# Kernel tuning notes

Measured on AMD Instinct MI355X. Metric: run time of the kernel, lower is better.

## Reference

```python
import jax, jax.numpy as jnp
import numpy as np

V, E, H = 32000, 256, 512   # vocab, embed_dim, hidden_dim
B, S, T = 16, 512, 128      # batch, src_len, tgt_len
PAD = 0
H2 = 2 * H                  # decoder hidden size


def setup_inputs() -> dict:
    key = jax.random.key(0)
    ks = jax.random.split(key, 20)
    g = lambda k, shape: jax.random.normal(k, shape, dtype=jnp.float32) * 0.05
    emb = g(ks[0], (V, E)).at[PAD].set(0.0)  # padding_idx row zeroed
    inp = {
        "src": jax.random.randint(ks[18], (B, S), 0, V, dtype=jnp.int32),
        "tgt": jax.random.randint(ks[19], (B, T), 0, V, dtype=jnp.int32),
        "emb": emb,
        # encoder forward direction (torch gate order i,f,g,o)
        "Wih_f": g(ks[1], (4 * H, E)), "Whh_f": g(ks[2], (4 * H, H)),
        "bih_f": g(ks[3], (4 * H,)),   "bhh_f": g(ks[4], (4 * H,)),
        # encoder backward direction
        "Wih_b": g(ks[5], (4 * H, E)), "Whh_b": g(ks[6], (4 * H, H)),
        "bih_b": g(ks[7], (4 * H,)),   "bhh_b": g(ks[8], (4 * H,)),
        # decoder LSTM: input E+2H, hidden 2H
        "Wih_d": g(ks[9], (4 * H2, E + H2)), "Whh_d": g(ks[10], (4 * H2, H2)),
        "bih_d": g(ks[11], (4 * H2,)),       "bhh_d": g(ks[12], (4 * H2,)),
        # attention Linear(4H -> 2H)
        "Wa": g(ks[13], (H2, 2 * H2)), "ba": g(ks[14], (H2,)),
        # output Linear(2H -> V)
        "Wo": g(ks[15], (V, H2)), "bo": g(ks[16], (V,)),
    }
    return inp


def _lstm_cell(x, h, c, Wih, Whh, bih, bhh):
    z = x @ Wih.T + h @ Whh.T + bih + bhh
    i, f, g, o = jnp.split(z, 4, axis=-1)
    c = jax.nn.sigmoid(f) * c + jax.nn.sigmoid(i) * jnp.tanh(g)
    h = jax.nn.sigmoid(o) * jnp.tanh(c)
    return h, c


def _lstm_scan(xs, h0, c0, Wih, Whh, bih, bhh):
    def step(carry, x):
        h, c = _lstm_cell(x, carry[0], carry[1], Wih, Whh, bih, bhh)
        return (h, c), h
    (hT, cT), hs = jax.lax.scan(step, (h0, c0), xs)
    return hs, hT, cT


def reference(src, tgt, emb, Wih_f, Whh_f, bih_f, bhh_f, Wih_b, Whh_b, bih_b, bhh_b,
              Wih_d, Whh_d, bih_d, bhh_d, Wa, ba, Wo, bo):
    z = jnp.zeros((B, H), dtype=emb.dtype)
    xs = emb[src].transpose(1, 0, 2)                       # [S,B,E]
    hs_f, hTf, _ = _lstm_scan(xs,        z, z, Wih_f, Whh_f, bih_f, bhh_f)
    hs_b, hTb, _ = _lstm_scan(xs[::-1],  z, z, Wih_b, Whh_b, bih_b, bhh_b)
    enc_out = jnp.concatenate([hs_f, hs_b[::-1]], -1).transpose(1, 0, 2)  # [B,S,2H]
    h = jnp.concatenate([hTf, hTb], -1)                    # decoder h0 [B,2H]
    c = jnp.zeros_like(h)  # note: original reuses encoder c_n; see combined c0 below
    # original uses c_n (last cells) as decoder c0:
    _, _, cTf = _lstm_scan(xs, z, z, Wih_f, Whh_f, bih_f, bhh_f)[1], None, None
    # recompute cleanly (scan already returned cT above; redo properly):
    hs_f2, hTf2, cTf2 = _lstm_scan(xs,       z, z, Wih_f, Whh_f, bih_f, bhh_f)
    hs_b2, hTb2, cTb2 = _lstm_scan(xs[::-1], z, z, Wih_b, Whh_b, bih_b, bhh_b)
    c = jnp.concatenate([cTf2, cTb2], -1)

    Wa_h, Wa_e = Wa[:, :H2], Wa[:, H2:]
    enc_proj = jnp.einsum('bsd,kd->bsk', enc_out, Wa_e) + ba  # [B,S,2H]

    dec_xs = emb[tgt[:, :T - 1]].transpose(1, 0, 2)        # [T-1,B,E] teacher-forced

    def dec_step(carry, x):
        h, c = carry
        energy = jnp.tanh(enc_proj + (h @ Wa_h.T)[:, None, :])  # [B,S,2H]
        w = jax.nn.softmax(energy.sum(-1), axis=1)              # [B,S]
        ctx = jnp.einsum('bs,bsd->bd', w, enc_out)              # [B,2H]
        xi = jnp.concatenate([x, ctx], -1)                      # [B,E+2H]
        h, c = _lstm_cell(xi, h, c, Wih_d, Whh_d, bih_d, bhh_d)
        pred = h @ Wo.T + bo                                    # [B,V]
        return (h, c), pred

    _, preds = jax.lax.scan(dec_step, (h, c), dec_xs)           # [T-1,B,V]
    outputs = jnp.concatenate(
        [jnp.zeros((B, 1, V), dtype=preds.dtype), preds.transpose(1, 0, 2)], axis=1)
    return outputs
```

## Files before the change

### kernel.cpp

```cpp
#include <hip/hip_runtime.h>

typedef unsigned int uint;
typedef unsigned short ushort;
typedef unsigned long long ull;
typedef __attribute__((ext_vector_type(8))) short bf16x8;
typedef __attribute__((ext_vector_type(4))) float f32x4;

static constexpr int V_ = 32000, E_ = 256, H_ = 512, B_ = 16, S_ = 512, T_ = 128;
static constexpr int H2_ = 1024, G4_ = 2048, D4_ = 4096, KXI_ = 2304;
static constexpr int DSTEPS = T_ - 1;
static constexpr int MD = 2048;
static constexpr int NWG_DEC = 256;
static constexpr float LOG2E = 1.4426950408889634f;
static constexpr int ASTR = 2312;

#define DEVFN __device__ __forceinline__

DEVFN ushort f2bf(float f){ uint u = __builtin_bit_cast(uint, f); u += 0x7fffu + ((u>>16)&1u); return (ushort)(u>>16); }
DEVFN float bf2f(ushort h){ uint u = ((uint)h)<<16; return __builtin_bit_cast(float, u); }
DEVFN float fsig(float x){ float e = __builtin_amdgcn_exp2f(-LOG2E*x); return __builtin_amdgcn_rcpf(1.f+e); }
DEVFN float ftanh(float x){ x = fminf(15.f,fmaxf(-15.f,x)); float e = __builtin_amdgcn_exp2f(2.f*LOG2E*x); return (e-1.f)*__builtin_amdgcn_rcpf(e+1.f); }
DEVFN f32x4 mfma16(bf16x8 a, bf16x8 b, f32x4 c){ return __builtin_amdgcn_mfma_f32_16x16x32_bf16(a,b,c,0,0,0); }

struct ull2v{ ull x, y; };
DEVFN ull ald64(const void* p){ return __hip_atomic_load((const ull*)p, __ATOMIC_RELAXED, __HIP_MEMORY_SCOPE_AGENT); }
DEVFN uint ald32u(const uint* p){ return __hip_atomic_load(p, __ATOMIC_RELAXED, __HIP_MEMORY_SCOPE_AGENT); }
DEVFN float ald_f32(const float* p){ uint v = __hip_atomic_load((const uint*)p, __ATOMIC_RELAXED, __HIP_MEMORY_SCOPE_AGENT); return __builtin_bit_cast(float, v); }
DEVFN bf16x8 ald_bf16x8(const ushort* p){ ull2v v{ald64(p), ald64(p+4)}; return __builtin_bit_cast(bf16x8, v); }
DEVFN void ast32(float* p, float v){ __hip_atomic_store(p, v, __ATOMIC_RELAXED, __HIP_MEMORY_SCOPE_AGENT); }
DEVFN void ast16(ushort* p, ushort v){ __hip_atomic_store(p, v, __ATOMIC_RELAXED, __HIP_MEMORY_SCOPE_AGENT); }
DEVFN void astu(uint* p, uint v){ __hip_atomic_store(p, v, __ATOMIC_RELAXED, __HIP_MEMORY_SCOPE_AGENT); }

DEVFN void gbar(uint* flags, int wgid, int tid, uint& rnd){
  __syncthreads();
  rnd++;
  if (tid==0) astu(flags + wgid, rnd);
  if (tid<256){
    while (ald32u(flags + tid) < rnd) __builtin_amdgcn_s_sleep(1);
  }
  __syncthreads();
}
DEVFN void lbar(uint* lflags, int grp, int mem, int tid, uint& rnd){
  __syncthreads();
  rnd++;
  if (tid==0) astu(lflags + grp*16 + mem, rnd);
  if (tid<16){
    while (ald32u(lflags + grp*16 + tid) < rnd) __builtin_amdgcn_s_sleep(1);
  }
  __syncthreads();
}

__global__ void k_init(uint* __restrict__ flags, ushort* __restrict__ hgf, ushort* __restrict__ hgb,
                       uint* __restrict__ hU, uint* __restrict__ ctxU){
  int i = blockIdx.x*256 + threadIdx.x;
  if (i < 1024) flags[i] = 0;
  if (i < 2*B_*H_){ hgf[i]=0; hgb[i]=0; }
  if (i < B_*H2_){ hU[i] = 0u; ctxU[i] = 0u; }
}

__global__ void k_embed(const int* __restrict__ src, const int* __restrict__ tgt,
                        const float* __restrict__ emb, ushort* __restrict__ Xb, ushort* __restrict__ DXb){
  int r = blockIdx.x, tid = threadIdx.x;
  if (r < S_*B_){
    int s = r>>4, b = r&15;
    int id = src[b*S_+s];
    Xb[(size_t)r*E_+tid] = f2bf(emb[(size_t)id*E_+tid]);
  } else {
    int r2 = r - S_*B_;
    int t = r2>>4, b = r2&15;
    int id = tgt[b*T_+t];
    DXb[(size_t)r2*E_+tid] = f2bf(emb[(size_t)id*E_+tid]);
  }
}

__global__ void k_cvt_encw(const float* __restrict__ src, ushort* __restrict__ dst){
  int d = blockIdx.x;
  int wg = d>>7, r = d&127;
  int w = r>>4, jj=(r>>2)&3, g=r&3;
  int srow = g*H_ + wg*32 + w*4 + jj;
  for (int c = threadIdx.x; c < E_; c += 256)
    dst[(size_t)d*E_ + c] = f2bf(src[(size_t)srow*E_ + c]);
}

__global__ void k_bias_encp(const float* __restrict__ bih, const float* __restrict__ bhh, float* __restrict__ dst){
  int d = blockIdx.x*256 + threadIdx.x;
  int wg = d>>7, r = d&127;
  int w = r>>4, jj=(r>>2)&3, g=r&3;
  int srow = g*H_ + wg*32 + w*4 + jj;
  dst[d] = bih[srow]+bhh[srow];
}

__global__ void k_cvt_decw(const float* __restrict__ Wih_d, const float* __restrict__ Whh_d,
                           ushort* __restrict__ dst){
  int d = blockIdx.x;
  int wg = d>>4, r = d&15, jj = r>>2, g = r&3;
  int srow = g*H2_ + wg*4 + jj;
  for (int c = threadIdx.x; c < KXI_; c += 256){
    float v = (c < E_+H2_) ? Wih_d[(size_t)srow*(E_+H2_) + c] : Whh_d[(size_t)srow*H2_ + (c - (E_+H2_))];
    dst[(size_t)d*KXI_ + c] = f2bf(v);
  }
}

__global__ void k_bias_decp(const float* __restrict__ bih, const float* __restrict__ bhh, float* __restrict__ dst){
  int d = blockIdx.x*256 + threadIdx.x;
  int wg = d>>4, r = d&15, jj = r>>2, g = r&3;
  int srow = g*H2_ + wg*4 + jj;
  dst[d] = bih[srow]+bhh[srow];
}

__global__ void k_cvt_strided(const float* __restrict__ src, ushort* __restrict__ dst,
                              int cols, int sld, int soff, int dld, int doff){
  int r = blockIdx.x;
  for (int c = threadIdx.x; c < cols; c += 256)
    dst[(size_t)r*dld + doff + c] = f2bf(src[(size_t)r*sld + soff + c]);
}

__global__ void k_zero_t0(float* __restrict__ out){
  int i = blockIdx.x*256 + threadIdx.x;
  if (i < B_*V_){ int b = i / V_, v = i - b*V_; out[(size_t)b*T_*V_ + v] = 0.f; }
}

template<int MODE>
__global__ __launch_bounds__(256) void gemm128(const ushort* __restrict__ A, const ushort* __restrict__ Bm,
    const float* __restrict__ bias, void* __restrict__ outp, int M, int N, int K, int Mvalid){
  __shared__ __align__(16) ushort As[128*32];
  __shared__ __align__(16) ushort Bs[128*32];
  int tid = threadIdx.x;
  int wave = tid>>6, lane = tid&63;
  int m0 = blockIdx.y*128, n0 = blockIdx.x*128;
  int wm = wave>>1, wn = wave&1;
  int col = lane&15, rg = lane>>4;
  f32x4 acc[4][4];
  #pragma unroll
  for (int i=0;i<4;i++)
    #pragma unroll
    for (int j=0;j<4;j++) acc[i][j] = {0.f,0.f,0.f,0.f};
  for (int k0=0;k0<K;k0+=32){
    __syncthreads();
    #pragma unroll
    for (int j=0;j<2;j++){
      int li = j*256+tid;
      int row = li>>2, ko = (li&3)*8;
      *(bf16x8*)(As + li*8) = *(const bf16x8*)(A + (size_t)(m0+row)*K + k0 + ko);
      *(bf16x8*)(Bs + li*8) = *(const bf16x8*)(Bm + (size_t)(n0+row)*K + k0 + ko);
    }
    __syncthreads();
    bf16x8 af[4], bfr[4];
    #pragma unroll
    for (int f=0;f<4;f++){
      af[f]  = *(const bf16x8*)(As + (wm*64+f*16+col)*32 + rg*8);
      bfr[f] = *(const bf16x8*)(Bs + (wn*64+f*16+col)*32 + rg*8);
    }
    #pragma unroll
    for (int fm=0;fm<4;fm++)
      #pragma unroll
      for (int fn=0;fn<4;fn++)
        acc[fm][fn] = mfma16(af[fm], bfr[fn], acc[fm][fn]);
  }
  #pragma unroll
  for (int fm=0;fm<4;fm++){
    int mrow = m0 + wm*64 + fm*16 + rg*4;
    #pragma unroll
    for (int fn=0;fn<4;fn++){
      int gcol = n0 + wn*64 + fn*16 + col;
      float bv = bias ? bias[gcol] : 0.f;
      #pragma unroll
      for (int i=0;i<4;i++){
        float v = acc[fm][fn][i] + bv;
        int grow = mrow + i;
        if (MODE==0) ((float*)outp)[(size_t)grow*N + gcol] = v;
        else if (MODE==1) ((ushort*)outp)[(size_t)grow*N + gcol] = f2bf(v);
        else if (MODE==3) ((ushort*)outp)[(size_t)(grow>>4)*(16*2048) + gcol*16 + (grow&15)] = f2bf(v);
        else { if (grow < Mvalid){ int b = grow&15, t = grow>>4;
               ((float*)outp)[(size_t)b*T_*V_ + (size_t)(t+1)*V_ + gcol] = v; } }
      }
    }
  }
}

__global__ __launch_bounds__(512) void k_enc_persist(
    const ushort* __restrict__ Xgf, const ushort* __restrict__ Xgb,
    const float* __restrict__ Whhf, const float* __restrict__ Whhb,
    ushort* __restrict__ enc, ushort* __restrict__ enct,
    uint* __restrict__ hbuf1, float* __restrict__ cbuf0,
    ushort* __restrict__ hgf, ushort* __restrict__ hgb,
    uint* __restrict__ flags){
  const int dir = blockIdx.x >> 4;
  const int wg  = blockIdx.x & 15;
  const ushort* Xg = dir ? Xgb : Xgf;
  const float* Whh = dir ? Whhb : Whhf;
  ushort* hg = dir ? hgb : hgf;
  uint* ef = flags + 512 + dir*16;
  __shared__ __align__(16) ushort Wlds[128*512];
  __shared__ __align__(16) ushort hls[16*512];
  int tid = threadIdx.x;
  for (int it=0; it<32; ++it){
    int r = it*4 + (tid>>7), ct = tid&127;
    int w_ = r>>4, jj=(r>>2)&3, g=r&3;
    int srow = g*H_ + wg*32 + w_*4 + jj;
    float4 v = *(const float4*)(Whh + (size_t)srow*H_ + ct*4);
    ushort4 o; o.x=f2bf(v.x); o.y=f2bf(v.y); o.z=f2bf(v.z); o.w=f2bf(v.w);
    int byte = (r*1024 + ct*8) ^ ((r&7)<<4);
    *(ushort4*)((char*)Wlds + byte) = o;
  }
  int w = tid>>6, lane = tid&63, colL = lane&15, rg = lane>>4;
  int gg = colL&3;
  uint rnd = 0;
  float cst[4];
  #pragma unroll
  for (int i=0;i<4;i++) cst[i]=0.f;
  __syncthreads();
  for (int t=0;t<S_;++t){
    int pos = dir ? (S_-1-t) : t;
    const ushort* hsrc = hg + (t&1)*B_*H_;
    bf16x8 hv[2];
    #pragma unroll
    for (int k2=0;k2<2;k2++){
      int idx = tid + k2*512;
      hv[k2] = ald_bf16x8(hsrc + (idx>>6)*H_ + (idx&63)*8);
    }
    int colg = wg*128 + w*16 + colL;
    ushort4 xv = *(const ushort4*)(Xg + ((size_t)pos*2048 + colg)*16 + rg*4);
    f32x4 acc;
    acc[0]=bf2f(xv.x); acc[1]=bf2f(xv.y); acc[2]=bf2f(xv.z); acc[3]=bf2f(xv.w);
    #pragma unroll
    for (int k2=0;k2<2;k2++){
      int idx = tid + k2*512;
      int byte = ((idx>>6)*1024 + (idx&63)*16) ^ (((idx>>6)&7)<<4);
      *(bf16x8*)((char*)hls + byte) = hv[k2];
    }
    __syncthreads();
    int rowb = w*16 + colL;
    int base = rowb*1024 + rg*16, xm = (rowb&7)<<4;
    int hbase = colL*1024 + rg*16, hxm = (colL&7)<<4;
    #pragma unroll
    for (int kt=0;kt<16;kt++){
      bf16x8 afv = *(const bf16x8*)((const char*)hls + ((hbase + kt*64) ^ hxm));
      bf16x8 bfv = *(const bf16x8*)((const char*)Wlds + ((base + kt*64) ^ xm));
      acc = mfma16(afv, bfv, acc);
    }
    ushort* hdst = hg + ((t+1)&1)*B_*H_;
    #pragma unroll
    for (int i=0;i<4;i++){
      float v0 = acc[i];
      float v1 = __shfl_xor(v0, 1);
      float v2 = __shfl_xor(v0, 2);
      float v3 = __shfl_xor(v1, 2);
      float zi = gg==0?v0: gg==1?v1: gg==2?v2: v3;
      float zf = (gg^1)==0?v0: (gg^1)==1?v1: (gg^1)==2?v2: v3;
      float zg = (gg^2)==0?v0: (gg^2)==1?v1: (gg^2)==2?v2: v3;
      float zo = (gg^3)==0?v0: (gg^3)==1?v1: (gg^3)==2?v2: v3;
      float cc = fsig(zf)*cst[i] + fsig(zi)*ftanh(zg);
      cst[i] = cc;
      float h = fsig(zo)*ftanh(cc);
      if (gg==0){
        int j = wg*32 + w*4 + (colL>>2);
        int b = rg*4+i;
        ushort hb = f2bf(h);
        enc[((size_t)b*S_ + pos)*H2_ + dir*H_ + j] = hb;
        enct[((size_t)b*H2_ + dir*H_ + j)*S_ + pos] = hb;
        ast16(&hdst[b*H_ + j], hb);
        if (t==S_-1){
          hbuf1[b*H2_ + dir*H_ + j] = (uint)hb;
          cbuf0[b*H2_ + dir*H_ + j] = cc;
        }
      }
    }
    if (t != S_-1){
      __syncthreads();
      rnd++;
      if (tid==0) astu(ef + wg, rnd);
      if (tid<16){
        while (ald32u(ef + tid) < rnd) __builtin_amdgcn_s_sleep(1);
      }
      __syncthreads();
    }
  }
}

__global__ __launch_bounds__(512) void k_dec(
    const float* __restrict__ P, const ushort* __restrict__ WaH,
    const ushort* __restrict__ Wd, const float* __restrict__ bsd,
    const ushort* __restrict__ enct, const ushort* __restrict__ DXb,
    const float* __restrict__ cbuf0, uint* __restrict__ hU,
    uint* __restrict__ ctxU, float* __restrict__ qbuf,
    float* __restrict__ scores, ushort* __restrict__ hsd,
    uint* __restrict__ flags){
  __shared__ __align__(16) ushort AB[16*ASTR];
  __shared__ __align__(16) float pr[8*256];
  __shared__ float redz[256];
  __shared__ float qls[1024];
  __shared__ float wls[512];
  __shared__ float part[512];
  __shared__ float red[16];
  __shared__ float cst[64];
  uint* lflags = flags + 256;
  int wgid = blockIdx.x, tid = threadIdx.x;
  int w = tid>>6, lane = tid&63, colL = lane&15, rg = lane>>4;
  int b = wgid>>4, wc = wgid&15;
  uint rnd = 0;
  if (tid < 64){
    int jj = tid>>4, b4 = tid&15;
    cst[tid] = cbuf0[b4*H2_ + wgid*4 + jj];
  }
  for (int st=0; st<DSTEPS; ++st){
    const uint* hprevU = hU + ((st+1)&1)*B_*H2_;
    const uint wantH = (uint)st;
    const uint wantC = (uint)(st+1);
    float* qslot = qbuf + (st&1)*B_*H2_;
    if (wgid >= 64 && wgid < 128){
      int n0 = (wgid-64)*16;
      const uint* hp = hprevU + colL*H2_ + w*128 + rg*8;
      uint uu[32];
      for(;;){
        #pragma unroll
        for (int kt=0;kt<4;kt++)
          #pragma unroll
          for (int j=0;j<4;j++){
            ull v = ald64(hp + kt*32 + j*2);
            uu[kt*8+j*2] = (uint)v; uu[kt*8+j*2+1] = (uint)(v>>32);
          }
        bool ok = true;
        #pragma unroll
        for (int i2=0;i2<32;i2++) ok &= ((uu[i2]>>16) == wantH);
        if (ok) break;
        __builtin_amdgcn_s_sleep(1);
      }
      f32x4 acc = {0.f,0.f,0.f,0.f};
      const ushort* Bp = WaH + (size_t)(n0+colL)*H2_ + w*128 + rg*8;
      #pragma unroll
      for (int kt=0;kt<4;kt++){
        ushort tmp[8];
        #pragma unroll
        for (int j=0;j<8;j++) tmp[j] = (ushort)uu[kt*8+j];
        acc = mfma16(*(bf16x8*)tmp, *(const bf16x8*)(Bp + kt*32), acc);
      }
      *(f32x4*)&pr[w*256 + lane*4] = acc;
      __syncthreads();
      if (tid < 256){
        float s = pr[tid];
        #pragma unroll
        for (int w8=1;w8<8;w8++) s += pr[w8*256 + tid];
        int l = tid>>2, i = tid&3;
        ast32(&qslot[(size_t)((l>>4)*4 + i)*H2_ + n0 + (l&15)], s);
      }
    }
    gbar(flags, wgid, tid, rnd);
    {
      ull q2 = ald64((const ull*)(qslot + (size_t)b*H2_) + tid);
      *(ull*)&qls[tid*2] = q2;
      __syncthreads();
      f32x4 qv[4];
      #pragma unroll
      for (int u=0;u<4;u++) qv[u] = *(const f32x4*)&qls[lane*16 + u*4];
      int rbase = b*S_ + wc*32 + w*4;
      #pragma unroll
      for (int rr=0;rr<4;rr++){
        int r = rbase + rr;
        const float4* Pr = (const float4*)(P + (size_t)r*H2_) + lane*4;
        float s = 0.f;
        #pragma unroll
        for (int u=0;u<4;u++){
          float4 pv = Pr[u];
          s += ftanh(pv.x+qv[u][0])+ftanh(pv.y+qv[u][1])+ftanh(pv.z+qv[u][2])+ftanh(pv.w+qv[u][3]);
        }
        #pragma unroll
        for (int o=32;o;o>>=1) s += __shfl_xor(s,o);
        if (lane==0) ast32(&scores[r], s);
      }
    }
    lbar(lflags, b, wc, tid, rnd);
    {
      float sc = ald_f32(scores + b*S_ + tid);
      float m = sc;
      #pragma unroll
      for (int o=32;o;o>>=1) m = fmaxf(m, __shfl_xor(m,o));
      if (lane==0) red[w] = m;
      __syncthreads();
      m = red[0];
      #pragma unroll
      for (int k2=1;k2<8;k2++) m = fmaxf(m, red[k2]);
      float e = __builtin_amdgcn_exp2f((sc - m)*LOG2E);
      float ss = e;
      #pragma unroll
      for (int o=32;o;o>>=1) ss += __shfl_xor(ss,o);
      if (lane==0) red[8+w] = ss;
      __syncthreads();
      float tot = red[8];
      #pragma unroll
      for (int k2=9;k2<16;k2++) tot += red[k2];
      wls[tid] = e * __builtin_amdgcn_rcpf(tot);
      __syncthreads();
      int c = wc*64 + (tid&63), sseg = tid>>6;
      const ushort* ep = enct + ((size_t)b*H2_ + c)*S_ + sseg*64;
      float a = 0.f;
      #pragma unroll
      for (int u=0;u<8;u++){
        bf16x8 ev = *(const bf16x8*)(ep + u*8);
        #pragma unroll
        for (int j=0;j<8;j++) a += wls[sseg*64 + u*8 + j] * bf2f((ushort)ev[j]);
      }
      part[tid] = a;
      __syncthreads();
      if (tid < 64){
        float s = part[tid];
        #pragma unroll
        for (int g2=1;g2<8;g2++) s += part[g2*64 + tid];
        astu(&ctxU[b*H2_ + wc*64 + tid], (uint)f2bf(s) | (wantC<<16));
      }
    }
    {
      { int b3 = tid>>5, seg = tid&31;
        *(bf16x8*)&AB[b3*ASTR + seg*8] = *(const bf16x8*)(DXb + (size_t)(st*16+b3)*E_ + seg*8); }
      {
        uint uu[32];
        for(;;){
          #pragma unroll
          for (int k2=0;k2<4;k2++){
            int idx = tid + k2*512;
            const uint* p = ctxU + (idx>>7)*H2_ + (idx&127)*8;
            #pragma unroll
            for (int j=0;j<4;j++){
              ull v = ald64(p + j*2);
              uu[k2*8+j*2] = (uint)v; uu[k2*8+j*2+1] = (uint)(v>>32);
            }
          }
          bool ok = true;
          #pragma unroll
          for (int i2=0;i2<32;i2++) ok &= ((uu[i2]>>16) == wantC);
          if (ok) break;
          __builtin_amdgcn_s_sleep(1);
        }
        #pragma unroll
        for (int k2=0;k2<4;k2++){
          int idx = tid + k2*512;
          ushort tmp[8];
          #pragma unroll
          for (int j=0;j<8;j++) tmp[j] = (ushort)uu[k2*8+j];
          *(bf16x8*)&AB[(idx>>7)*ASTR + 256 + (idx&127)*8] = *(bf16x8*)tmp;
        }
      }
      {
        uint uu[32];
        for(;;){
          #pragma unroll
          for (int k2=0;k2<4;k2++){
            int idx = tid + k2*512;
            const uint* p = hprevU + (idx>>7)*H2_ + (idx&127)*8;
            #pragma unroll
            for (int j=0;j<4;j++){
              ull v = ald64(p + j*2);
              uu[k2*8+j*2] = (uint)v; uu[k2*8+j*2+1] = (uint)(v>>32);
            }
          }
          bool ok = true;
          #pragma unroll
          for (int i2=0;i2<32;i2++) ok &= ((uu[i2]>>16) == wantH);
          if (ok) break;
          __builtin_amdgcn_s_sleep(1);
        }
        #pragma unroll
        for (int k2=0;k2<4;k2++){
          int idx = tid + k2*512;
          ushort tmp[8];
          #pragma unroll
          for (int j=0;j<8;j++) tmp[j] = (ushort)uu[k2*8+j];
          *(bf16x8*)&AB[(idx>>7)*ASTR + 1280 + (idx&127)*8] = *(bf16x8*)tmp;
        }
      }
      __syncthreads();
      int row0 = wgid*16;
      f32x4 acc = {0.f,0.f,0.f,0.f};
      const ushort* Bp = Wd + (size_t)(row0+colL)*KXI_ + w*288 + rg*8;
      const ushort* Apb = &AB[colL*ASTR + w*288 + rg*8];
      #pragma unroll
      for (int kt=0;kt<9;kt++)
        acc = mfma16(*(const bf16x8*)(Apb + kt*32), *(const bf16x8*)(Bp + kt*32), acc);
      *(f32x4*)&pr[w*256 + lane*4] = acc;
      __syncthreads();
      if (tid < 256){
        float s = bsd[row0 + ((tid>>2)&15)];
        #pragma unroll
        for (int w8=0;w8<8;w8++) s += pr[w8*256 + tid];
        redz[tid] = s;
      }
      __syncthreads();
      if (tid < 64){
        int jj = tid>>4, b4 = tid&15, rgc = b4>>2, ic = b4&3;
        float zi = redz[((jj*4+0) + 16*rgc)*4 + ic];
        float zf = redz[((jj*4+1) + 16*rgc)*4 + ic];
        float zg = redz[((jj*4+2) + 16*rgc)*4 + ic];
        float zo = redz[((jj*4+3) + 16*rgc)*4 + ic];
        float cc2 = fsig(zf)*cst[tid] + fsig(zi)*ftanh(zg);
        cst[tid] = cc2;
        float h = fsig(zo)*ftanh(cc2);
        ushort hb = f2bf(h);
        int j = wgid*4 + jj;
        astu(&hU[(st&1)*B_*H2_ + b4*H2_ + j], (uint)hb | ((uint)(st+1)<<16));
        hsd[((size_t)st*B_ + b4)*H2_ + j] = hb;
      }
      __syncthreads();
    }
  }
}

extern "C" void kernel_launch(void* const* d_in, const int* in_sizes, int n_in,
                              void* d_out, int out_size, void* d_ws, size_t ws_size,
                              hipStream_t stream) {
  const int* src   = (const int*)d_in[0];
  const int* tgt   = (const int*)d_in[1];
  const float* emb   = (const float*)d_in[2];
  const float* Wih_f = (const float*)d_in[3];
  const float* Whh_f = (const float*)d_in[4];
  const float* bih_f = (const float*)d_in[5];
  const float* bhh_f = (const float*)d_in[6];
  const float* Wih_b = (const float*)d_in[7];
  const float* Whh_b = (const float*)d_in[8];
  const float* bih_b = (const float*)d_in[9];
  const float* bhh_b = (const float*)d_in[10];
  const float* Wih_d = (const float*)d_in[11];
  const float* Whh_d = (const float*)d_in[12];
  const float* bih_d = (const float*)d_in[13];
  const float* bhh_d = (const float*)d_in[14];
  const float* Wa    = (const float*)d_in[15];
  const float* ba    = (const float*)d_in[16];
  const float* Wo    = (const float*)d_in[17];
  const float* bo    = (const float*)d_in[18];
  float* out = (float*)d_out;
  (void)in_sizes; (void)n_in; (void)out_size; (void)ws_size;

  char* ws = (char*)d_ws;
  size_t off = 0;
  auto alloc = [&](size_t bytes)->char*{ char* p = ws + off; off += (bytes + 255) & ~(size_t)255; return p; };
  ushort* Xb     = (ushort*)alloc((size_t)S_*B_*E_*2);
  ushort* DXb    = (ushort*)alloc((size_t)DSTEPS*B_*E_*2);
  ushort* Wihf_p = (ushort*)alloc((size_t)G4_*E_*2);
  ushort* Wihb_p = (ushort*)alloc((size_t)G4_*E_*2);
  float*  bsf    = (float*)alloc(G4_*4);
  float*  bsb    = (float*)alloc(G4_*4);
  ushort* ENC    = (ushort*)alloc((size_t)B_*S_*H2_*2);
  ushort* ENCT   = (ushort*)alloc((size_t)B_*S_*H2_*2);
  ushort* WaH    = (ushort*)alloc((size_t)H2_*H2_*2);
  ushort* WaE    = (ushort*)alloc((size_t)H2_*H2_*2);
  ushort* Wd     = (ushort*)alloc((size_t)D4_*KXI_*2);
  float*  bsd    = (float*)alloc(D4_*4);
  ushort* WoB    = (ushort*)alloc((size_t)V_*H2_*2);
  float*  cbuf0  = (float*)alloc(B_*H2_*4);
  uint*   hU     = (uint*)alloc((size_t)2*B_*H2_*4);
  uint*   ctxU   = (uint*)alloc((size_t)B_*H2_*4);
  float*  qbuf   = (float*)alloc((size_t)2*B_*H2_*4);
  float*  scores = (float*)alloc(B_*S_*4);
  ushort* hsd    = (ushort*)alloc((size_t)MD*H2_*2);
  ushort* hgf    = (ushort*)alloc((size_t)2*B_*H_*2);
  ushort* hgb    = (ushort*)alloc((size_t)2*B_*H_*2);
  uint*   flags  = (uint*)alloc(4096);
  char*   big    = alloc((size_t)2*S_*B_*G4_*2);
  ushort* Xgf = (ushort*)big;
  ushort* Xgb = (ushort*)(big + (size_t)S_*B_*G4_*2);
  float*  P   = (float*)big;

  k_init<<<dim3(64), dim3(256), 0, stream>>>(flags, hgf, hgb, hU, ctxU);
  k_embed<<<dim3(S_*B_ + DSTEPS*B_), dim3(E_), 0, stream>>>(src, tgt, emb, Xb, DXb);
  k_cvt_encw<<<dim3(G4_), dim3(256), 0, stream>>>(Wih_f, Wihf_p);
  k_cvt_encw<<<dim3(G4_), dim3(256), 0, stream>>>(Wih_b, Wihb_p);
  k_bias_encp<<<dim3(8), dim3(256), 0, stream>>>(bih_f, bhh_f, bsf);
  k_bias_encp<<<dim3(8), dim3(256), 0, stream>>>(bih_b, bhh_b, bsb);
  k_cvt_strided<<<dim3(H2_), dim3(256), 0, stream>>>(Wa, WaH, H2_, 2*H2_, 0,   H2_, 0);
  k_cvt_strided<<<dim3(H2_), dim3(256), 0, stream>>>(Wa, WaE, H2_, 2*H2_, H2_, H2_, 0);
  k_cvt_decw<<<dim3(D4_), dim3(256), 0, stream>>>(Wih_d, Whh_d, Wd);
  k_bias_decp<<<dim3(16), dim3(256), 0, stream>>>(bih_d, bhh_d, bsd);
  k_cvt_strided<<<dim3(V_),  dim3(256), 0, stream>>>(Wo, WoB, H2_, H2_, 0, H2_, 0);

  gemm128<3><<<dim3(G4_/128, (S_*B_)/128), dim3(256), 0, stream>>>(Xb, Wihf_p, bsf, Xgf, S_*B_, G4_, E_, 0);
  gemm128<3><<<dim3(G4_/128, (S_*B_)/128), dim3(256), 0, stream>>>(Xb, Wihb_p, bsb, Xgb, S_*B_, G4_, E_, 0);

  k_enc_persist<<<dim3(32), dim3(512), 0, stream>>>(Xgf, Xgb, Whh_f, Whh_b, ENC, ENCT,
                                                    hU + B_*H2_, cbuf0, hgf, hgb, flags);

  gemm128<0><<<dim3(H2_/128, (B_*S_)/128), dim3(256), 0, stream>>>(ENC, WaE, ba, P, B_*S_, H2_, H2_, 0);
  k_zero_t0<<<dim3((B_*V_+255)/256), dim3(256), 0, stream>>>(out);

  k_dec<<<dim3(NWG_DEC), dim3(512), 0, stream>>>(P, WaH, Wd, bsd, ENCT, DXb, cbuf0, hU,
                                                 ctxU, qbuf, scores, hsd, flags);

  gemm128<2><<<dim3(V_/128, MD/128), dim3(256), 0, stream>>>(hsd, WoB, bo, out, MD, V_, H2_, DSTEPS*B_);
}
```

Before: 6.039 ms.

## Replace step barriers with tagged-data polling in encoder and decoder

The encoder stops using a flag barrier across its 16 workgroups after every step. Each hidden value is now stored as a 32-bit word holding the step number in its upper half, and consumers poll until every word they read carries the expected tag. In the decoder, the full 256-workgroup barrier after the query projection is replaced by waiting only on the 64 producer workgroups' flags, and the context buffer is double-buffered so a slot can be reused safely. This removes global barrier round-trips on the serial critical path, at the cost of doubling the hidden-state traffic and adding spin-polling on data.

```diff
diff --git a/kernel.cpp b/kernel.cpp
--- a/kernel.cpp
+++ b/kernel.cpp
@@ -26,20 +26,10 @@
 DEVFN ull ald64(const void* p){ return __hip_atomic_load((const ull*)p, __ATOMIC_RELAXED, __HIP_MEMORY_SCOPE_AGENT); }
 DEVFN uint ald32u(const uint* p){ return __hip_atomic_load(p, __ATOMIC_RELAXED, __HIP_MEMORY_SCOPE_AGENT); }
 DEVFN float ald_f32(const float* p){ uint v = __hip_atomic_load((const uint*)p, __ATOMIC_RELAXED, __HIP_MEMORY_SCOPE_AGENT); return __builtin_bit_cast(float, v); }
-DEVFN bf16x8 ald_bf16x8(const ushort* p){ ull2v v{ald64(p), ald64(p+4)}; return __builtin_bit_cast(bf16x8, v); }
 DEVFN void ast32(float* p, float v){ __hip_atomic_store(p, v, __ATOMIC_RELAXED, __HIP_MEMORY_SCOPE_AGENT); }
 DEVFN void ast16(ushort* p, ushort v){ __hip_atomic_store(p, v, __ATOMIC_RELAXED, __HIP_MEMORY_SCOPE_AGENT); }
 DEVFN void astu(uint* p, uint v){ __hip_atomic_store(p, v, __ATOMIC_RELAXED, __HIP_MEMORY_SCOPE_AGENT); }
 
-DEVFN void gbar(uint* flags, int wgid, int tid, uint& rnd){
-  __syncthreads();
-  rnd++;
-  if (tid==0) astu(flags + wgid, rnd);
-  if (tid<256){
-    while (ald32u(flags + tid) < rnd) __builtin_amdgcn_s_sleep(1);
-  }
-  __syncthreads();
-}
 DEVFN void lbar(uint* lflags, int grp, int mem, int tid, uint& rnd){
   __syncthreads();
   rnd++;
@@ -50,12 +40,13 @@
   __syncthreads();
 }
 
-__global__ void k_init(uint* __restrict__ flags, ushort* __restrict__ hgf, ushort* __restrict__ hgb,
+__global__ void k_init(uint* __restrict__ flags, uint* __restrict__ hgf, uint* __restrict__ hgb,
                        uint* __restrict__ hU, uint* __restrict__ ctxU){
   int i = blockIdx.x*256 + threadIdx.x;
   if (i < 1024) flags[i] = 0;
-  if (i < 2*B_*H_){ hgf[i]=0; hgb[i]=0; }
-  if (i < B_*H2_){ hU[i] = 0u; ctxU[i] = 0u; }
+  if (i < 2*B_*H_){ hgf[i]=0u; hgb[i]=0u; }
+  if (i < B_*H2_) hU[i] = 0u;
+  if (i < 2*B_*H2_) ctxU[i] = 0u;
 }
 
 __global__ void k_embed(const int* __restrict__ src, const int* __restrict__ tgt,
@@ -183,14 +174,12 @@
     const float* __restrict__ Whhf, const float* __restrict__ Whhb,
     ushort* __restrict__ enc, ushort* __restrict__ enct,
     uint* __restrict__ hbuf1, float* __restrict__ cbuf0,
-    ushort* __restrict__ hgf, ushort* __restrict__ hgb,
-    uint* __restrict__ flags){
+    uint* __restrict__ hgf, uint* __restrict__ hgb){
   const int dir = blockIdx.x >> 4;
   const int wg  = blockIdx.x & 15;
   const ushort* Xg = dir ? Xgb : Xgf;
   const float* Whh = dir ? Whhb : Whhf;
-  ushort* hg = dir ? hgb : hgf;
-  uint* ef = flags + 512 + dir*16;
+  uint* hg = dir ? hgb : hgf;
   __shared__ __align__(16) ushort Wlds[128*512];
   __shared__ __align__(16) ushort hls[16*512];
   int tid = threadIdx.x;
@@ -205,19 +194,30 @@
   }
   int w = tid>>6, lane = tid&63, colL = lane&15, rg = lane>>4;
   int gg = colL&3;
-  uint rnd = 0;
   float cst[4];
   #pragma unroll
   for (int i=0;i<4;i++) cst[i]=0.f;
   __syncthreads();
   for (int t=0;t<S_;++t){
     int pos = dir ? (S_-1-t) : t;
-    const ushort* hsrc = hg + (t&1)*B_*H_;
-    bf16x8 hv[2];
-    #pragma unroll
-    for (int k2=0;k2<2;k2++){
-      int idx = tid + k2*512;
-      hv[k2] = ald_bf16x8(hsrc + (idx>>6)*H_ + (idx&63)*8);
+    const uint* hsrcU = hg + (t&1)*B_*H_;
+    uint uu[16];
+    for(;;){
+      #pragma unroll
+      for (int k2=0;k2<2;k2++){
+        int idx = tid + k2*512;
+        const uint* p = hsrcU + (idx>>6)*H_ + (idx&63)*8;
+        #pragma unroll
+        for (int j=0;j<4;j++){
+          ull v = ald64(p + j*2);
+          uu[k2*8+j*2] = (uint)v; uu[k2*8+j*2+1] = (uint)(v>>32);
+        }
+      }
+      bool ok = true;
+      #pragma unroll
+      for (int i2=0;i2<16;i2++) ok &= ((uu[i2]>>16) == (uint)t);
+      if (ok) break;
+      __builtin_amdgcn_s_sleep(1);
     }
     int colg = wg*128 + w*16 + colL;
     ushort4 xv = *(const ushort4*)(Xg + ((size_t)pos*2048 + colg)*16 + rg*4);
@@ -227,7 +227,10 @@
     for (int k2=0;k2<2;k2++){
       int idx = tid + k2*512;
       int byte = ((idx>>6)*1024 + (idx&63)*16) ^ (((idx>>6)&7)<<4);
-      *(bf16x8*)((char*)hls + byte) = hv[k2];
+      ushort tmp[8];
+      #pragma unroll
+      for (int j=0;j<8;j++) tmp[j] = (ushort)uu[k2*8+j];
+      *(bf16x8*)((char*)hls + byte) = *(bf16x8*)tmp;
     }
     __syncthreads();
     int rowb = w*16 + colL;
@@ -239,7 +242,7 @@
       bf16x8 bfv = *(const bf16x8*)((const char*)Wlds + ((base + kt*64) ^ xm));
       acc = mfma16(afv, bfv, acc);
     }
-    ushort* hdst = hg + ((t+1)&1)*B_*H_;
+    uint* hdstU = hg + ((t+1)&1)*B_*H_;
     #pragma unroll
     for (int i=0;i<4;i++){
       float v0 = acc[i];
@@ -259,22 +262,14 @@
         ushort hb = f2bf(h);
         enc[((size_t)b*S_ + pos)*H2_ + dir*H_ + j] = hb;
         enct[((size_t)b*H2_ + dir*H_ + j)*S_ + pos] = hb;
-        ast16(&hdst[b*H_ + j], hb);
+        astu(&hdstU[b*H_ + j], (uint)hb | ((uint)(t+1)<<16));
         if (t==S_-1){
           hbuf1[b*H2_ + dir*H_ + j] = (uint)hb;
           cbuf0[b*H2_ + dir*H_ + j] = cc;
         }
       }
     }
-    if (t != S_-1){
-      __syncthreads();
-      rnd++;
-      if (tid==0) astu(ef + wg, rnd);
-      if (tid<16){
-        while (ald32u(ef + tid) < rnd) __builtin_amdgcn_s_sleep(1);
-      }
-      __syncthreads();
-    }
+    __syncthreads();
   }
 }
 
@@ -295,6 +290,7 @@
   __shared__ float red[16];
   __shared__ float cst[64];
   uint* lflags = flags + 256;
+  uint* qf     = flags + 768;
   int wgid = blockIdx.x, tid = threadIdx.x;
   int w = tid>>6, lane = tid&63, colL = lane&15, rg = lane>>4;
   int b = wgid>>4, wc = wgid&15;
@@ -305,6 +301,7 @@
   }
   for (int st=0; st<DSTEPS; ++st){
     const uint* hprevU = hU + ((st+1)&1)*B_*H2_;
+    uint* cslot = ctxU + (st&1)*B_*H2_;
     const uint wantH = (uint)st;
     const uint wantC = (uint)(st+1);
     float* qslot = qbuf + (st&1)*B_*H2_;
@@ -344,8 +341,13 @@
         int l = tid>>2, i = tid&3;
         ast32(&qslot[(size_t)((l>>4)*4 + i)*H2_ + n0 + (l&15)], s);
       }
-    }
-    gbar(flags, wgid, tid, rnd);
+      __syncthreads();
+      if (tid==0) astu(qf + (wgid-64), wantC);
+    }
+    if (tid < 64){
+      while (ald32u(qf + tid) < wantC) __builtin_amdgcn_s_sleep(1);
+    }
+    __syncthreads();
     {
       ull q2 = ald64((const ull*)(qslot + (size_t)b*H2_) + tid);
       *(ull*)&qls[tid*2] = q2;
@@ -406,7 +408,7 @@
         float s = part[tid];
         #pragma unroll
         for (int g2=1;g2<8;g2++) s += part[g2*64 + tid];
-        astu(&ctxU[b*H2_ + wc*64 + tid], (uint)f2bf(s) | (wantC<<16));
+        astu(&cslot[b*H2_ + wc*64 + tid], (uint)f2bf(s) | (wantC<<16));
       }
     }
     {
@@ -418,7 +420,7 @@
           #pragma unroll
           for (int k2=0;k2<4;k2++){
             int idx = tid + k2*512;
-            const uint* p = ctxU + (idx>>7)*H2_ + (idx&127)*8;
+            const uint* p = cslot + (idx>>7)*H2_ + (idx&127)*8;
             #pragma unroll
             for (int j=0;j<4;j++){
               ull v = ald64(p + j*2);
@@ -547,19 +549,19 @@
   ushort* WoB    = (ushort*)alloc((size_t)V_*H2_*2);
   float*  cbuf0  = (float*)alloc(B_*H2_*4);
   uint*   hU     = (uint*)alloc((size_t)2*B_*H2_*4);
-  uint*   ctxU   = (uint*)alloc((size_t)B_*H2_*4);
+  uint*   ctxU   = (uint*)alloc((size_t)2*B_*H2_*4);
   float*  qbuf   = (float*)alloc((size_t)2*B_*H2_*4);
   float*  scores = (float*)alloc(B_*S_*4);
   ushort* hsd    = (ushort*)alloc((size_t)MD*H2_*2);
-  ushort* hgf    = (ushort*)alloc((size_t)2*B_*H_*2);
-  ushort* hgb    = (ushort*)alloc((size_t)2*B_*H_*2);
+  uint*   hgf    = (uint*)alloc((size_t)2*B_*H_*4);
+  uint*   hgb    = (uint*)alloc((size_t)2*B_*H_*4);
   uint*   flags  = (uint*)alloc(4096);
   char*   big    = alloc((size_t)2*S_*B_*G4_*2);
   ushort* Xgf = (ushort*)big;
   ushort* Xgb = (ushort*)(big + (size_t)S_*B_*G4_*2);
   float*  P   = (float*)big;
 
-  k_init<<<dim3(64), dim3(256), 0, stream>>>(flags, hgf, hgb, hU, ctxU);
+  k_init<<<dim3(128), dim3(256), 0, stream>>>(flags, hgf, hgb, hU, ctxU);
   k_embed<<<dim3(S_*B_ + DSTEPS*B_), dim3(E_), 0, stream>>>(src, tgt, emb, Xb, DXb);
   k_cvt_encw<<<dim3(G4_), dim3(256), 0, stream>>>(Wih_f, Wihf_p);
   k_cvt_encw<<<dim3(G4_), dim3(256), 0, stream>>>(Wih_b, Wihb_p);
@@ -575,7 +577,7 @@
   gemm128<3><<<dim3(G4_/128, (S_*B_)/128), dim3(256), 0, stream>>>(Xb, Wihb_p, bsb, Xgb, S_*B_, G4_, E_, 0);
 
   k_enc_persist<<<dim3(32), dim3(512), 0, stream>>>(Xgf, Xgb, Whh_f, Whh_b, ENC, ENCT,
-                                                    hU + B_*H2_, cbuf0, hgf, hgb, flags);
+                                                    hU + B_*H2_, cbuf0, hgf, hgb);
 
   gemm128<0><<<dim3(H2_/128, (B_*S_)/128), dim3(256), 0, stream>>>(ENC, WaE, ba, P, B_*S_, H2_, H2_, 0);
   k_zero_t0<<<dim3((B_*V_+255)/256), dim3(256), 0, stream>>>(out);
```

Result: faster. 5.800 ms (-4.0%).
